# Kernel optimization log

Hardware: AMD Instinct MI355X
Metric: run time of the kernel (lower is better)

Reference implementation:

```python
import jax, jax.numpy as jnp
import numpy as np

NEG_SLOPE = 0.2  # GATConv attention leaky_relu slope (init arg)
POST_SLOPE = 0.2  # leaky_relu after LayerNorm in outer forward
N_LAYERS = 3


def _leaky(x, slope):
    return jnp.where(x >= 0, x, slope * x)


def _layer_norm(x, g, b):
    mu = jnp.mean(x, axis=-1, keepdims=True)
    var = jnp.var(x, axis=-1, keepdims=True)
    return (x - mu) * jax.lax.rsqrt(var + 1e-5) * g + b


def _gat_conv(h, W, al, ar, bias, src, dst, apply_act):
    # DGL GATConv (eval mode, dropout = identity)
    N = h.shape[0]
    H, D = al.shape
    feat = (h @ W).reshape(N, H, D)                      # [N,H,D]
    el = jnp.einsum('nhd,hd->nh', feat, al)              # [N,H]
    er = jnp.einsum('nhd,hd->nh', feat, ar)              # [N,H]
    e = _leaky(el[src] + er[dst], NEG_SLOPE)             # [E,H] edge logits
    # segment (per-destination) softmax, numerically stable
    m = jax.ops.segment_max(e, dst, num_segments=N)      # [N,H]
    ex = jnp.exp(e - m[dst])                             # [E,H]
    s = jax.ops.segment_sum(ex, dst, num_segments=N)     # [N,H]
    alpha = ex / s[dst]                                  # [E,H]
    msg = alpha[:, :, None] * feat[src]                  # [E,H,D]
    rst = jax.ops.segment_sum(msg, dst, num_segments=N)  # [N,H,D]
    rst = rst + bias.reshape(1, H, D)
    if apply_act:
        rst = jax.nn.elu(rst)
    return rst


def setup_inputs() -> dict:
    key = jax.random.key(0)
    ks = jax.random.split(key, 12)
    N, E, IN, D, H, C = 100000, 1600000, 256, 64, 4, 40
    HID = H * D  # 256
    sc = 0.05
    return {
        'x': jax.random.normal(ks[0], (N, IN), jnp.float32),
        'W_h': jax.random.normal(ks[1], (3, IN, HID), jnp.float32) * sc,
        'attn_l_h': jax.random.normal(ks[2], (3, H, D), jnp.float32) * sc,
        'attn_r_h': jax.random.normal(ks[3], (3, H, D), jnp.float32) * sc,
        'bias_h': jnp.zeros((3, HID), jnp.float32),
        'ln_g': jnp.ones((3, HID), jnp.float32),
        'ln_b': jnp.zeros((3, HID), jnp.float32),
        'W_o': jax.random.normal(ks[4], (HID, C), jnp.float32) * sc,
        'attn_l_o': jax.random.normal(ks[5], (1, C), jnp.float32) * sc,
        'attn_r_o': jax.random.normal(ks[6], (1, C), jnp.float32) * sc,
        'bias_o': jnp.zeros((C,), jnp.float32),
        'edge_src': jax.random.randint(ks[7], (E,), 0, N, jnp.int32),
        'edge_dst': jax.random.randint(ks[8], (E,), 0, N, jnp.int32),
    }


def reference(x, W_h, attn_l_h, attn_r_h, bias_h, ln_g, ln_b,
              W_o, attn_l_o, attn_r_o, bias_o, edge_src, edge_dst):
    h = x
    for l in range(N_LAYERS):
        hn = _gat_conv(h, W_h[l], attn_l_h[l], attn_r_h[l], bias_h[l],
                       edge_src, edge_dst, True)
        hn = hn.reshape(hn.shape[0], -1)          # flatten heads -> [N, H*D]
        hn = _layer_norm(hn, ln_g[l], ln_b[l])
        hn = _leaky(hn, POST_SLOPE)
        h = hn + h if h.shape == hn.shape else hn  # residual when shapes match
    logits = _gat_conv(h, W_o, attn_l_o, attn_r_o, bias_o,
                       edge_src, edge_dst, False).sum(axis=1)  # sum over heads
    return logits
```

## Files before the change

### kernel.cpp

```cpp
#include <hip/hip_runtime.h>
#include <math.h>


#define NEG_SLOPE 0.2f

typedef __attribute__((ext_vector_type(8))) short bf16x8;
typedef __attribute__((ext_vector_type(4))) float floatx4;

__device__ __forceinline__ float leaky(float x) { return x >= 0.f ? x : NEG_SLOPE * x; }

__device__ __forceinline__ unsigned short f2bf(float f) {
    unsigned u = __builtin_bit_cast(unsigned, f);
    u += 0x7fffu + ((u >> 16) & 1u);
    return (unsigned short)(u >> 16);
}
__device__ __forceinline__ float bf2f(unsigned short h) {
    unsigned u = ((unsigned)h) << 16;
    return __builtin_bit_cast(float, u);
}

__global__ void zero_i32(int* __restrict__ p, int n) {
    int i = blockIdx.x * blockDim.x + threadIdx.x;
    if (i < n) p[i] = 0;
}

__global__ void hist_kernel(const int* __restrict__ dst, int* __restrict__ counts, int E) {
    int e = blockIdx.x * blockDim.x + threadIdx.x;
    if (e < E) atomicAdd(&counts[dst[e]], 1);
}

__global__ void alloc_kernel(const int* __restrict__ counts, int* __restrict__ start,
                             int* __restrict__ cursor, int* __restrict__ total, int N) {
    int n = blockIdx.x * blockDim.x + threadIdx.x;
    if (n < N) {
        int c = counts[n];
        int s = atomicAdd(total, c);
        start[n] = s;
        cursor[n] = s;
    }
}

__global__ void scatter_kernel(const int* __restrict__ src, const int* __restrict__ dst,
                               int* __restrict__ cursor, int* __restrict__ col, int E) {
    int e = blockIdx.x * blockDim.x + threadIdx.x;
    if (e < E) {
        int p = atomicAdd(&cursor[dst[e]], 1);
        col[p] = src[e];
    }
}

__global__ void convert_bf(const float* __restrict__ src, unsigned short* __restrict__ dst,
                           int n4) {
    int i = blockIdx.x * blockDim.x + threadIdx.x;
    if (i < n4) {
        float4 v = *(const float4*)(src + (size_t)i * 4);
        ushort4 s;
        s.x = f2bf(v.x); s.y = f2bf(v.y); s.z = f2bf(v.z); s.w = f2bf(v.w);
        *(ushort4*)(dst + (size_t)i * 4) = s;
    }
}

__global__ void transpose_w(const float* __restrict__ W, unsigned short* __restrict__ Wt) {
    int idx = blockIdx.x * 256 + threadIdx.x;
    int l = idx >> 16, r = idx & 65535;
    int k = r >> 8, n = r & 255;
    Wt[l * 65536 + n * 256 + k] = f2bf(W[l * 65536 + k * 256 + n]);
}

__global__ void transpose_wo(const float* __restrict__ W, unsigned short* __restrict__ Wt) {
    int idx = blockIdx.x * 256 + threadIdx.x;
    int n = idx >> 8, k = idx & 255;
    Wt[n * 256 + k] = (n < 40) ? f2bf(W[k * 40 + n]) : (unsigned short)0;
}

#define LDSK 40
__global__ __launch_bounds__(256, 2) void gemm_bf16(const unsigned short* __restrict__ A,
                                                    const unsigned short* __restrict__ Wt,
                                                    unsigned short* __restrict__ Cb, int M) {
    __shared__ unsigned short As[128 * LDSK];
    __shared__ unsigned short Bs[128 * LDSK];
    const int tid = threadIdx.x;
    const int bx = blockIdx.x & 1;
    const int by = blockIdx.x >> 1;
    const int row0 = by * 128, col0 = bx * 128;
    const int lane = tid & 63, wid = tid >> 6;
    const int wm = (wid & 1) * 64, wn = (wid >> 1) * 64;

    floatx4 acc[4][4] = {};

    for (int kb = 0; kb < 256; kb += 32) {
#pragma unroll
        for (int i = 0; i < 2; ++i) {
            int idx = tid + 256 * i;
            int r = idx >> 2, k8 = (idx & 3) * 8;
            int gr = row0 + r;
            bf16x8 v = {};
            if (gr < M) v = *(const bf16x8*)(A + (size_t)gr * 256 + kb + k8);
            *(bf16x8*)&As[r * LDSK + k8] = v;
            int n = col0 + r;
            *(bf16x8*)&Bs[r * LDSK + k8] = *(const bf16x8*)(Wt + (size_t)n * 256 + kb + k8);
        }
        __syncthreads();
        const int q = lane >> 4, m = lane & 15;
        bf16x8 af[4], bfr[4];
#pragma unroll
        for (int i = 0; i < 4; ++i) {
            af[i] = *(const bf16x8*)&As[(wm + i * 16 + m) * LDSK + q * 8];
            bfr[i] = *(const bf16x8*)&Bs[(wn + i * 16 + m) * LDSK + q * 8];
        }
#pragma unroll
        for (int i = 0; i < 4; ++i)
#pragma unroll
            for (int j = 0; j < 4; ++j)
                acc[i][j] = __builtin_amdgcn_mfma_f32_16x16x32_bf16(af[i], bfr[j], acc[i][j], 0, 0, 0);
        __syncthreads();
    }

    const int q = lane >> 4, c = lane & 15;
#pragma unroll
    for (int i = 0; i < 4; ++i)
#pragma unroll
        for (int j = 0; j < 4; ++j)
#pragma unroll
            for (int r = 0; r < 4; ++r) {
                int grow = row0 + wm + i * 16 + q * 4 + r;
                int gcol = col0 + wn + j * 16 + c;
                if (grow < M) Cb[(size_t)grow * 256 + gcol] = f2bf(acc[i][j][r]);
            }
}

#define BSTRIDE 264
__global__ __launch_bounds__(256) void gemm_out_mfma(const unsigned short* __restrict__ h,
                                                     const unsigned short* __restrict__ Wt,
                                                     unsigned short* __restrict__ feat_o, int N) {
    __shared__ unsigned short As[128 * LDSK];
    __shared__ unsigned short Bs[48 * BSTRIDE];
    const int tid = threadIdx.x;
    const int row0 = blockIdx.x * 128;
    const int lane = tid & 63, wid = tid >> 6;

#pragma unroll
    for (int i = 0; i < 6; ++i) {
        int f = tid + 256 * i;
        int n = f >> 5, kk = (f & 31) * 8;
        *(bf16x8*)&Bs[n * BSTRIDE + kk] = *(const bf16x8*)(Wt + n * 256 + kk);
    }
    __syncthreads();

    floatx4 acc[2][3] = {};
    for (int kb = 0; kb < 256; kb += 32) {
#pragma unroll
        for (int i = 0; i < 2; ++i) {
            int idx = tid + 256 * i;
            int r = idx >> 2, k8 = (idx & 3) * 8;
            int gr = row0 + r;
            bf16x8 v = {};
            if (gr < N) v = *(const bf16x8*)(h + (size_t)gr * 256 + kb + k8);
            *(bf16x8*)&As[r * LDSK + k8] = v;
        }
        __syncthreads();
        const int q = lane >> 4, m = lane & 15;
        bf16x8 af[2], bfr[3];
#pragma unroll
        for (int i = 0; i < 2; ++i)
            af[i] = *(const bf16x8*)&As[(wid * 32 + i * 16 + m) * LDSK + q * 8];
#pragma unroll
        for (int j = 0; j < 3; ++j)
            bfr[j] = *(const bf16x8*)&Bs[(j * 16 + m) * BSTRIDE + kb + q * 8];
#pragma unroll
        for (int i = 0; i < 2; ++i)
#pragma unroll
            for (int j = 0; j < 3; ++j)
                acc[i][j] = __builtin_amdgcn_mfma_f32_16x16x32_bf16(af[i], bfr[j], acc[i][j], 0, 0, 0);
        __syncthreads();
    }

    const int q = lane >> 4, c = lane & 15;
#pragma unroll
    for (int i = 0; i < 2; ++i)
#pragma unroll
        for (int j = 0; j < 3; ++j)
#pragma unroll
            for (int r = 0; r < 4; ++r) {
                int grow = row0 + wid * 32 + i * 16 + q * 4 + r;
                int gcol = j * 16 + c;
                if (grow < N && gcol < 40) feat_o[(size_t)grow * 40 + gcol] = f2bf(acc[i][j][r]);
            }
}

__global__ __launch_bounds__(256) void scores_out(const unsigned short* __restrict__ feat_o,
                                                  const float* __restrict__ alo,
                                                  const float* __restrict__ aro,
                                                  float* __restrict__ elo,
                                                  float* __restrict__ ero, int N) {
    int node = blockIdx.x * 4 + (threadIdx.x >> 6);
    int lane = threadIdx.x & 63;
    if (node >= N) return;
    float v = 0.f, a = 0.f, r = 0.f;
    if (lane < 40) {
        v = bf2f(feat_o[(size_t)node * 40 + lane]);
        a = alo[lane];
        r = aro[lane];
    }
    float pl = v * a, pr = v * r;
#pragma unroll
    for (int off = 32; off >= 1; off >>= 1) {
        pl += __shfl_xor(pl, off);
        pr += __shfl_xor(pr, off);
    }
    if (lane == 0) {
        elo[node] = pl;
        ero[node] = pr;
    }
}

__global__ __launch_bounds__(256) void scores_bf(const unsigned short* __restrict__ feat,
                                                 const float* __restrict__ al,
                                                 const float* __restrict__ ar,
                                                 float* __restrict__ el,
                                                 float* __restrict__ er, int N) {
    int node = blockIdx.x * 4 + (threadIdx.x >> 6);
    int lane = threadIdx.x & 63;
    if (node >= N) return;
    ushort4 u = *(const ushort4*)(feat + (size_t)node * 256 + lane * 4);
    float4 a = *(const float4*)(al + lane * 4);
    float4 r = *(const float4*)(ar + lane * 4);
    float f0 = bf2f(u.x), f1 = bf2f(u.y), f2 = bf2f(u.z), f3 = bf2f(u.w);
    float pl = f0 * a.x + f1 * a.y + f2 * a.z + f3 * a.w;
    float pr = f0 * r.x + f1 * r.y + f2 * r.z + f3 * r.w;
#pragma unroll
    for (int off = 8; off >= 1; off >>= 1) {
        pl += __shfl_xor(pl, off);
        pr += __shfl_xor(pr, off);
    }
    if ((lane & 15) == 0) {
        int head = lane >> 4;
        el[node * 4 + head] = pl;
        er[node * 4 + head] = pr;
    }
}

__global__ __launch_bounds__(256) void aggregate_hidden(
    const unsigned short* __restrict__ feat, const float* __restrict__ el,
    const float* __restrict__ er, const int* __restrict__ start, const int* __restrict__ endp,
    const int* __restrict__ col, const float* __restrict__ bias, const float* __restrict__ lng,
    const float* __restrict__ lnb, const unsigned short* __restrict__ h_in,
    unsigned short* __restrict__ h_out, int N) {
    int node = blockIdx.x * 4 + (threadIdx.x >> 6);
    int lane = threadIdx.x & 63;
    if (node >= N) return;
    int begin = __builtin_amdgcn_readfirstlane(start[node]);
    int end = __builtin_amdgcn_readfirstlane(endp[node]);
    const int head = lane >> 4;
    const float erh = er[(size_t)node * 4 + head];

    const int ch = lane * 4;
    const unsigned short* fbase = feat + ch;
    const size_t hstr = 256;
    float4 acc = {0.f, 0.f, 0.f, 0.f};
    float ssum = 0.f;
    int e = begin;
    for (; e + 7 < end; e += 8) {
        int sA = col[e], sB = col[e + 1], sC = col[e + 2], sD = col[e + 3];
        int sE = col[e + 4], sF = col[e + 5], sG = col[e + 6], sH = col[e + 7];
        float eA = el[(size_t)sA * 4 + head];
        float eB = el[(size_t)sB * 4 + head];
        float eC = el[(size_t)sC * 4 + head];
        float eD = el[(size_t)sD * 4 + head];
        float eE = el[(size_t)sE * 4 + head];
        float eF = el[(size_t)sF * 4 + head];
        float eG = el[(size_t)sG * 4 + head];
        float eH = el[(size_t)sH * 4 + head];
        ushort4 uA = *(const ushort4*)(fbase + sA * hstr);
        ushort4 uB = *(const ushort4*)(fbase + sB * hstr);
        ushort4 uC = *(const ushort4*)(fbase + sC * hstr);
        ushort4 uD = *(const ushort4*)(fbase + sD * hstr);
        ushort4 uE = *(const ushort4*)(fbase + sE * hstr);
        ushort4 uF = *(const ushort4*)(fbase + sF * hstr);
        ushort4 uG = *(const ushort4*)(fbase + sG * hstr);
        ushort4 uH = *(const ushort4*)(fbase + sH * hstr);
        float wA = __expf(leaky(eA + erh));
        float wB = __expf(leaky(eB + erh));
        float wC = __expf(leaky(eC + erh));
        float wD = __expf(leaky(eD + erh));
        float wE = __expf(leaky(eE + erh));
        float wF = __expf(leaky(eF + erh));
        float wG = __expf(leaky(eG + erh));
        float wH = __expf(leaky(eH + erh));
        ssum += wA + wB + wC + wD + wE + wF + wG + wH;
        acc.x = fmaf(wA, bf2f(uA.x), acc.x); acc.y = fmaf(wA, bf2f(uA.y), acc.y);
        acc.z = fmaf(wA, bf2f(uA.z), acc.z); acc.w = fmaf(wA, bf2f(uA.w), acc.w);
        acc.x = fmaf(wB, bf2f(uB.x), acc.x); acc.y = fmaf(wB, bf2f(uB.y), acc.y);
        acc.z = fmaf(wB, bf2f(uB.z), acc.z); acc.w = fmaf(wB, bf2f(uB.w), acc.w);
        acc.x = fmaf(wC, bf2f(uC.x), acc.x); acc.y = fmaf(wC, bf2f(uC.y), acc.y);
        acc.z = fmaf(wC, bf2f(uC.z), acc.z); acc.w = fmaf(wC, bf2f(uC.w), acc.w);
        acc.x = fmaf(wD, bf2f(uD.x), acc.x); acc.y = fmaf(wD, bf2f(uD.y), acc.y);
        acc.z = fmaf(wD, bf2f(uD.z), acc.z); acc.w = fmaf(wD, bf2f(uD.w), acc.w);
        acc.x = fmaf(wE, bf2f(uE.x), acc.x); acc.y = fmaf(wE, bf2f(uE.y), acc.y);
        acc.z = fmaf(wE, bf2f(uE.z), acc.z); acc.w = fmaf(wE, bf2f(uE.w), acc.w);
        acc.x = fmaf(wF, bf2f(uF.x), acc.x); acc.y = fmaf(wF, bf2f(uF.y), acc.y);
        acc.z = fmaf(wF, bf2f(uF.z), acc.z); acc.w = fmaf(wF, bf2f(uF.w), acc.w);
        acc.x = fmaf(wG, bf2f(uG.x), acc.x); acc.y = fmaf(wG, bf2f(uG.y), acc.y);
        acc.z = fmaf(wG, bf2f(uG.z), acc.z); acc.w = fmaf(wG, bf2f(uG.w), acc.w);
        acc.x = fmaf(wH, bf2f(uH.x), acc.x); acc.y = fmaf(wH, bf2f(uH.y), acc.y);
        acc.z = fmaf(wH, bf2f(uH.z), acc.z); acc.w = fmaf(wH, bf2f(uH.w), acc.w);
    }
    for (; e < end; ++e) {
        int sA = col[e];
        float wA = __expf(leaky(el[(size_t)sA * 4 + head] + erh));
        ushort4 uA = *(const ushort4*)(fbase + sA * hstr);
        ssum += wA;
        acc.x = fmaf(wA, bf2f(uA.x), acc.x); acc.y = fmaf(wA, bf2f(uA.y), acc.y);
        acc.z = fmaf(wA, bf2f(uA.z), acc.z); acc.w = fmaf(wA, bf2f(uA.w), acc.w);
    }
    float inv = ssum > 0.f ? 1.f / ssum : 0.f;
    acc.x *= inv; acc.y *= inv; acc.z *= inv; acc.w *= inv;

    float4 bb = *(const float4*)(bias + ch);
    float x0 = acc.x + bb.x, x1 = acc.y + bb.y, x2 = acc.z + bb.z, x3 = acc.w + bb.w;
    x0 = x0 > 0.f ? x0 : expm1f(x0);
    x1 = x1 > 0.f ? x1 : expm1f(x1);
    x2 = x2 > 0.f ? x2 : expm1f(x2);
    x3 = x3 > 0.f ? x3 : expm1f(x3);
    float lsum = x0 + x1 + x2 + x3;
    float lsq = x0 * x0 + x1 * x1 + x2 * x2 + x3 * x3;
#pragma unroll
    for (int off = 32; off >= 1; off >>= 1) {
        lsum += __shfl_xor(lsum, off);
        lsq += __shfl_xor(lsq, off);
    }
    float mu = lsum * (1.f / 256.f);
    float var = lsq * (1.f / 256.f) - mu * mu;
    float rstd = rsqrtf(var + 1e-5f);
    float4 g4 = *(const float4*)(lng + ch);
    float4 b4 = *(const float4*)(lnb + ch);
    ushort4 hi = *(const ushort4*)(h_in + (size_t)node * 256 + ch);
    float y0 = (x0 - mu) * rstd * g4.x + b4.x;
    float y1 = (x1 - mu) * rstd * g4.y + b4.y;
    float y2 = (x2 - mu) * rstd * g4.z + b4.z;
    float y3 = (x3 - mu) * rstd * g4.w + b4.w;
    y0 = (y0 >= 0.f ? y0 : 0.2f * y0) + bf2f(hi.x);
    y1 = (y1 >= 0.f ? y1 : 0.2f * y1) + bf2f(hi.y);
    y2 = (y2 >= 0.f ? y2 : 0.2f * y2) + bf2f(hi.z);
    y3 = (y3 >= 0.f ? y3 : 0.2f * y3) + bf2f(hi.w);
    ushort4 o;
    o.x = f2bf(y0); o.y = f2bf(y1); o.z = f2bf(y2); o.w = f2bf(y3);
    *(ushort4*)(h_out + (size_t)node * 256 + ch) = o;
}

__global__ __launch_bounds__(256) void aggregate_out(const unsigned short* __restrict__ feat_o,
                                                     const float* __restrict__ elo,
                                                     const float* __restrict__ ero,
                                                     const int* __restrict__ start,
                                                     const int* __restrict__ endp,
                                                     const int* __restrict__ col,
                                                     const float* __restrict__ bias_o,
                                                     float* __restrict__ out, int N) {
    int node = blockIdx.x * 4 + (threadIdx.x >> 6);
    int lane = threadIdx.x & 63;
    if (node >= N) return;
    int begin = __builtin_amdgcn_readfirstlane(start[node]);
    int end = __builtin_amdgcn_readfirstlane(endp[node]);
    float ern = ero[node];
    int cc = lane < 40 ? lane : 0;
    float acc = 0.f, ssum = 0.f;
    int e = begin;
    for (; e + 7 < end; e += 8) {
        int sA = col[e], sB = col[e + 1], sC = col[e + 2], sD = col[e + 3];
        int sE = col[e + 4], sF = col[e + 5], sG = col[e + 6], sH = col[e + 7];
        float eA = elo[sA], eB = elo[sB], eC = elo[sC], eD = elo[sD];
        float eE = elo[sE], eF = elo[sF], eG = elo[sG], eH = elo[sH];
        unsigned short fA = feat_o[(size_t)sA * 40 + cc];
        unsigned short fB = feat_o[(size_t)sB * 40 + cc];
        unsigned short fC = feat_o[(size_t)sC * 40 + cc];
        unsigned short fD = feat_o[(size_t)sD * 40 + cc];
        unsigned short fE = feat_o[(size_t)sE * 40 + cc];
        unsigned short fF = feat_o[(size_t)sF * 40 + cc];
        unsigned short fG = feat_o[(size_t)sG * 40 + cc];
        unsigned short fH = feat_o[(size_t)sH * 40 + cc];
        float wA = __expf(leaky(eA + ern));
        float wB = __expf(leaky(eB + ern));
        float wC = __expf(leaky(eC + ern));
        float wD = __expf(leaky(eD + ern));
        float wE = __expf(leaky(eE + ern));
        float wF = __expf(leaky(eF + ern));
        float wG = __expf(leaky(eG + ern));
        float wH = __expf(leaky(eH + ern));
        ssum += wA + wB + wC + wD + wE + wF + wG + wH;
        acc = fmaf(wA, bf2f(fA), acc);
        acc = fmaf(wB, bf2f(fB), acc);
        acc = fmaf(wC, bf2f(fC), acc);
        acc = fmaf(wD, bf2f(fD), acc);
        acc = fmaf(wE, bf2f(fE), acc);
        acc = fmaf(wF, bf2f(fF), acc);
        acc = fmaf(wG, bf2f(fG), acc);
        acc = fmaf(wH, bf2f(fH), acc);
    }
    for (; e < end; ++e) {
        int sA = col[e];
        float wA = __expf(leaky(elo[sA] + ern));
        ssum += wA;
        acc = fmaf(wA, bf2f(feat_o[(size_t)sA * 40 + cc]), acc);
    }
    float inv = ssum > 0.f ? 1.f / ssum : 0.f;
    if (lane < 40) out[(size_t)node * 40 + lane] = acc * inv + bias_o[lane];
}

extern "C" void kernel_launch(void* const* d_in, const int* in_sizes, int n_in,
                              void* d_out, int out_size, void* d_ws, size_t ws_size,
                              hipStream_t stream) {
    const float* x = (const float*)d_in[0];
    const float* W_h = (const float*)d_in[1];
    const float* al_h = (const float*)d_in[2];
    const float* ar_h = (const float*)d_in[3];
    const float* bias_h = (const float*)d_in[4];
    const float* ln_g = (const float*)d_in[5];
    const float* ln_b = (const float*)d_in[6];
    const float* W_o = (const float*)d_in[7];
    const float* al_o = (const float*)d_in[8];
    const float* ar_o = (const float*)d_in[9];
    const float* bias_o = (const float*)d_in[10];
    const int* esrc = (const int*)d_in[11];
    const int* edst = (const int*)d_in[12];
    const int N = in_sizes[0] / 256;
    const int E = in_sizes[11];
    float* out = (float*)d_out;

    char* ws = (char*)d_ws;
    size_t off = 0;
    auto walloc = [&](size_t bytes) -> void* {
        void* p = ws + off;
        off += (bytes + 255) & ~(size_t)255;
        return p;
    };
    unsigned short* x_bf = (unsigned short*)walloc((size_t)N * 256 * 2);
    unsigned short* h_bf = (unsigned short*)walloc((size_t)N * 256 * 2);
    unsigned short* feat_bf = (unsigned short*)walloc((size_t)N * 256 * 2);
    unsigned short* Wt = (unsigned short*)walloc((size_t)3 * 65536 * 2);
    unsigned short* Wt_o = (unsigned short*)walloc((size_t)48 * 256 * 2);
    float* el = (float*)walloc((size_t)N * 4 * 4);
    float* er = (float*)walloc((size_t)N * 4 * 4);
    int* counts = (int*)walloc(((size_t)N + 1) * 4);
    int* start = (int*)walloc((size_t)N * 4);
    int* endp = (int*)walloc((size_t)N * 4);
    int* col = (int*)walloc((size_t)E * 4);
    if (off > ws_size) return;

    const int TB = 256;
    convert_bf<<<(N * 64 + TB - 1) / TB, TB, 0, stream>>>(x, x_bf, N * 64);
    transpose_w<<<3 * 65536 / TB, TB, 0, stream>>>(W_h, Wt);
    transpose_wo<<<48, TB, 0, stream>>>(W_o, Wt_o);
    zero_i32<<<(N + 1 + TB - 1) / TB, TB, 0, stream>>>(counts, N + 1);
    hist_kernel<<<(E + TB - 1) / TB, TB, 0, stream>>>(edst, counts, E);
    alloc_kernel<<<(N + TB - 1) / TB, TB, 0, stream>>>(counts, start, endp, counts + N, N);
    scatter_kernel<<<(E + TB - 1) / TB, TB, 0, stream>>>(esrc, edst, endp, col, E);

    const int nb4 = (N + 3) / 4;
    const int gemm_grid = ((N + 127) / 128) * 2;
    for (int l = 0; l < 3; ++l) {
        const unsigned short* hin = (l == 0) ? x_bf : h_bf;
        gemm_bf16<<<gemm_grid, 256, 0, stream>>>(hin, Wt + (size_t)l * 65536, feat_bf, N);
        scores_bf<<<nb4, 256, 0, stream>>>(feat_bf, al_h + l * 256, ar_h + l * 256, el, er, N);
        aggregate_hidden<<<nb4, 256, 0, stream>>>(feat_bf, el, er, start, endp, col,
                                                  bias_h + l * 256, ln_g + l * 256,
                                                  ln_b + l * 256, hin, h_bf, N);
    }
    unsigned short* feat_o = feat_bf;
    float* elo = el;
    float* ero = er;
    gemm_out_mfma<<<(N + 127) / 128, 256, 0, stream>>>(h_bf, Wt_o, feat_o, N);
    scores_out<<<nb4, 256, 0, stream>>>(feat_o, al_o, ar_o, elo, ero, N);
    aggregate_out<<<nb4, 256, 0, stream>>>(feat_o, elo, ero, start, endp, col, bias_o, out, N);
}
```

Baseline: 1.045 ms.

## Fuse attention score computation into GEMM epilogue and prefetch next K tile

Result: faster. 1.017 ms (-2.7%).

```diff
diff --git a/kernel.cpp b/kernel.cpp
--- a/kernel.cpp
+++ b/kernel.cpp
@@ -74,9 +74,10 @@
 }
 
 #define LDSK 40
-__global__ __launch_bounds__(256, 2) void gemm_bf16(const unsigned short* __restrict__ A,
-                                                    const unsigned short* __restrict__ Wt,
-                                                    unsigned short* __restrict__ Cb, int M) {
+__global__ __launch_bounds__(256, 2) void gemm_bf16_fused(
+    const unsigned short* __restrict__ A, const unsigned short* __restrict__ Wt,
+    const float* __restrict__ al, const float* __restrict__ ar,
+    unsigned short* __restrict__ Cb, float* __restrict__ el, float* __restrict__ er, int M) {
     __shared__ unsigned short As[128 * LDSK];
     __shared__ unsigned short Bs[128 * LDSK];
     const int tid = threadIdx.x;
@@ -86,22 +87,33 @@
     const int lane = tid & 63, wid = tid >> 6;
     const int wm = (wid & 1) * 64, wn = (wid >> 1) * 64;
 
+    const int rA = tid >> 2, k8 = (tid & 3) * 8;
+    auto loadA = [&](int kb, int rr) -> bf16x8 {
+        int gr = row0 + rr;
+        bf16x8 v = {};
+        if (gr < M) v = *(const bf16x8*)(A + (size_t)gr * 256 + kb + k8);
+        return v;
+    };
+    auto loadB = [&](int kb, int rr) -> bf16x8 {
+        return *(const bf16x8*)(Wt + (size_t)(col0 + rr) * 256 + kb + k8);
+    };
+
     floatx4 acc[4][4] = {};
-
+    bf16x8 pa0 = loadA(0, rA), pa1 = loadA(0, rA + 64);
+    bf16x8 pb0 = loadB(0, rA), pb1 = loadB(0, rA + 64);
+
+    const int q = lane >> 4, m = lane & 15;
     for (int kb = 0; kb < 256; kb += 32) {
-#pragma unroll
-        for (int i = 0; i < 2; ++i) {
-            int idx = tid + 256 * i;
-            int r = idx >> 2, k8 = (idx & 3) * 8;
-            int gr = row0 + r;
-            bf16x8 v = {};
-            if (gr < M) v = *(const bf16x8*)(A + (size_t)gr * 256 + kb + k8);
-            *(bf16x8*)&As[r * LDSK + k8] = v;
-            int n = col0 + r;
-            *(bf16x8*)&Bs[r * LDSK + k8] = *(const bf16x8*)(Wt + (size_t)n * 256 + kb + k8);
+        *(bf16x8*)&As[rA * LDSK + k8] = pa0;
+        *(bf16x8*)&As[(rA + 64) * LDSK + k8] = pa1;
+        *(bf16x8*)&Bs[rA * LDSK + k8] = pb0;
+        *(bf16x8*)&Bs[(rA + 64) * LDSK + k8] = pb1;
+        __syncthreads();
+        int nkb = kb + 32;
+        if (nkb < 256) {
+            pa0 = loadA(nkb, rA); pa1 = loadA(nkb, rA + 64);
+            pb0 = loadB(nkb, rA); pb1 = loadB(nkb, rA + 64);
         }
-        __syncthreads();
-        const int q = lane >> 4, m = lane & 15;
         bf16x8 af[4], bfr[4];
 #pragma unroll
         for (int i = 0; i < 4; ++i) {
@@ -116,7 +128,7 @@
         __syncthreads();
     }
 
-    const int q = lane >> 4, c = lane & 15;
+    const int c = lane & 15;
 #pragma unroll
     for (int i = 0; i < 4; ++i)
 #pragma unroll
@@ -127,6 +139,31 @@
                 int gcol = col0 + wn + j * 16 + c;
                 if (grow < M) Cb[(size_t)grow * 256 + gcol] = f2bf(acc[i][j][r]);
             }
+
+    const int head = bx * 2 + (wn >> 6);
+    const float* alh = al + head * 64;
+    const float* arh = ar + head * 64;
+    float a0 = alh[c], a1 = alh[16 + c], a2 = alh[32 + c], a3 = alh[48 + c];
+    float r0 = arh[c], r1 = arh[16 + c], r2 = arh[32 + c], r3 = arh[48 + c];
+#pragma unroll
+    for (int i = 0; i < 4; ++i)
+#pragma unroll
+        for (int r = 0; r < 4; ++r) {
+            float pel = acc[i][0][r] * a0 + acc[i][1][r] * a1 + acc[i][2][r] * a2 + acc[i][3][r] * a3;
+            float per = acc[i][0][r] * r0 + acc[i][1][r] * r1 + acc[i][2][r] * r2 + acc[i][3][r] * r3;
+#pragma unroll
+            for (int off = 8; off >= 1; off >>= 1) {
+                pel += __shfl_xor(pel, off);
+                per += __shfl_xor(per, off);
+            }
+            if (c == 0) {
+                int grow = row0 + wm + i * 16 + q * 4 + r;
+                if (grow < M) {
+                    el[(size_t)grow * 4 + head] = pel;
+                    er[(size_t)grow * 4 + head] = per;
+                }
+            }
+        }
 }
 
 #define BSTRIDE 264
@@ -211,32 +248,6 @@
     if (lane == 0) {
         elo[node] = pl;
         ero[node] = pr;
-    }
-}
-
-__global__ __launch_bounds__(256) void scores_bf(const unsigned short* __restrict__ feat,
-                                                 const float* __restrict__ al,
-                                                 const float* __restrict__ ar,
-                                                 float* __restrict__ el,
-                                                 float* __restrict__ er, int N) {
-    int node = blockIdx.x * 4 + (threadIdx.x >> 6);
-    int lane = threadIdx.x & 63;
-    if (node >= N) return;
-    ushort4 u = *(const ushort4*)(feat + (size_t)node * 256 + lane * 4);
-    float4 a = *(const float4*)(al + lane * 4);
-    float4 r = *(const float4*)(ar + lane * 4);
-    float f0 = bf2f(u.x), f1 = bf2f(u.y), f2 = bf2f(u.z), f3 = bf2f(u.w);
-    float pl = f0 * a.x + f1 * a.y + f2 * a.z + f3 * a.w;
-    float pr = f0 * r.x + f1 * r.y + f2 * r.z + f3 * r.w;
-#pragma unroll
-    for (int off = 8; off >= 1; off >>= 1) {
-        pl += __shfl_xor(pl, off);
-        pr += __shfl_xor(pr, off);
-    }
-    if ((lane & 15) == 0) {
-        int head = lane >> 4;
-        el[node * 4 + head] = pl;
-        er[node * 4 + head] = pr;
     }
 }
 
@@ -459,8 +470,9 @@
     const int gemm_grid = ((N + 127) / 128) * 2;
     for (int l = 0; l < 3; ++l) {
         const unsigned short* hin = (l == 0) ? x_bf : h_bf;
-        gemm_bf16<<<gemm_grid, 256, 0, stream>>>(hin, Wt + (size_t)l * 65536, feat_bf, N);
-        scores_bf<<<nb4, 256, 0, stream>>>(feat_bf, al_h + l * 256, ar_h + l * 256, el, er, N);
+        gemm_bf16_fused<<<gemm_grid, 256, 0, stream>>>(hin, Wt + (size_t)l * 65536,
+                                                       al_h + l * 256, ar_h + l * 256,
+                                                       feat_bf, el, er, N);
         aggregate_hidden<<<nb4, 256, 0, stream>>>(feat_bf, el, er, start, endp, col,
                                                   bias_h + l * 256, ln_g + l * 256,
                                                   ln_b + l * 256, hin, h_bf, N);
```
